# Optimization experiments

Measured on AMD Instinct MI355X. Metric: run time of the kernel, lower is better.

Reference implementation:

```python
import jax, jax.numpy as jnp
import numpy as np

CHANNELS, STYLE_DIM, N_HEADS, N_TOK = 512, 256, 2, 50
HEAD_DIM = STYLE_DIM // N_HEADS
SCALE = STYLE_DIM ** (-0.5)


def setup_inputs() -> dict:
    key = jax.random.key(0)
    ks = jax.random.split(key, 12)
    B, T = 16, 4096
    s = lambda fan_in: 1.0 / np.sqrt(fan_in)
    return {
        "x": jax.random.normal(ks[0], (B, CHANNELS, T), jnp.float32),
        "style": jax.random.normal(ks[1], (B, N_TOK, STYLE_DIM), jnp.float32),
        "key_emb": jax.random.normal(ks[2], (1, N_TOK, STYLE_DIM), jnp.float32) * 0.3,
        "Wq": jax.random.uniform(ks[3], (STYLE_DIM, CHANNELS), jnp.float32, -s(CHANNELS), s(CHANNELS)),
        "bq": jax.random.uniform(ks[4], (STYLE_DIM,), jnp.float32, -s(CHANNELS), s(CHANNELS)),
        "Wk": jax.random.uniform(ks[5], (STYLE_DIM, STYLE_DIM), jnp.float32, -s(STYLE_DIM), s(STYLE_DIM)),
        "bk": jax.random.uniform(ks[6], (STYLE_DIM,), jnp.float32, -s(STYLE_DIM), s(STYLE_DIM)),
        "Wv": jax.random.uniform(ks[7], (STYLE_DIM, STYLE_DIM), jnp.float32, -s(STYLE_DIM), s(STYLE_DIM)),
        "bv": jax.random.uniform(ks[8], (STYLE_DIM,), jnp.float32, -s(STYLE_DIM), s(STYLE_DIM)),
        "Wo": jax.random.uniform(ks[9], (CHANNELS, STYLE_DIM), jnp.float32, -s(STYLE_DIM), s(STYLE_DIM)),
        "bo": jax.random.uniform(ks[10], (CHANNELS,), jnp.float32, -s(STYLE_DIM), s(STYLE_DIM)),
    }


def reference(x, style, key_emb, Wq, bq, Wk, bk, Wv, bv, Wo, bo):
    B, C, T = x.shape
    N = style.shape[1]
    # Q from x (transposed to [B,T,C]); K from static learned embedding; V from style
    q = jnp.einsum('bct,dc->btd', x, Wq) + bq                 # [B,T,style_dim]
    k = jnp.einsum('bns,ds->bnd', jnp.broadcast_to(key_emb, (B, N_TOK, STYLE_DIM)), Wk) + bk
    v = jnp.einsum('bns,ds->bnd', style, Wv) + bv
    # split heads: [B,H,T,hd] / [B,H,N,hd]
    q = q.reshape(B, T, N_HEADS, HEAD_DIM).transpose(0, 2, 1, 3)
    k = k.reshape(B, N_TOK, N_HEADS, HEAD_DIM).transpose(0, 2, 1, 3)
    v = v.reshape(B, N, N_HEADS, HEAD_DIM).transpose(0, 2, 1, 3)
    # tanh applied to transposed keys before QK^T
    attn = jnp.einsum('bhtd,bhnd->bhtn', q, jnp.tanh(k)) * SCALE
    attn = jax.nn.softmax(attn, axis=-1)
    out = jnp.einsum('bhtn,bhnd->bhtd', attn, v)              # [B,H,T,hd]
    out = out.transpose(0, 2, 1, 3).reshape(B, T, STYLE_DIM)
    out = jnp.einsum('btd,cd->btc', out, Wo) + bo             # [B,T,C]
    return x + out.transpose(0, 2, 1)
```

## Files before the change

### kernel.cpp

```cpp
#include <hip/hip_runtime.h>
#include <stdint.h>

#define CHN 512
#define TDIM 4096
#define SD 256
#define HD 128
#define NTOK 50
#define NP 64
#define NB 16
#define TT 64
#define QPITCH 264
#define XPITCH 132
#define SCALE_ 0.0625f

typedef float f32x4 __attribute__((ext_vector_type(4)));
typedef unsigned int u32x4 __attribute__((ext_vector_type(4)));
typedef short s16x8 __attribute__((ext_vector_type(8)));

__device__ __forceinline__ uint16_t f2bf(float f) {
  union { float f; uint32_t u; } v; v.f = f;
  uint32_t r = (v.u + 0x7fffu + ((v.u >> 16) & 1u)) >> 16;
  return (uint16_t)r;
}
__device__ __forceinline__ uint32_t packbf(float lo, float hi) {
  return (uint32_t)f2bf(lo) | ((uint32_t)f2bf(hi) << 16);
}
__device__ __forceinline__ void mfma_bf16(f32x4& d, u32x4 a, u32x4 b) {
  union { u32x4 u; s16x8 s; } ua, ub;
  ua.u = a; ub.u = b;
  d = __builtin_amdgcn_mfma_f32_16x16x32_bf16(ua.s, ub.s, d, 0, 0, 0);
}

__global__ void conv_w_kernel(const float* __restrict__ Wq, const float* __restrict__ Wo,
                              uint16_t* __restrict__ wqb, uint16_t* __restrict__ wob) {
  int i = blockIdx.x * 256 + threadIdx.x;
  wqb[i] = f2bf(Wq[i]);
  wob[i] = f2bf(Wo[i]);
}

__global__ void prep_kv_kernel(const float* __restrict__ style, const float* __restrict__ kemb,
                               const float* __restrict__ Wk, const float* __restrict__ bk,
                               const float* __restrict__ Wv, const float* __restrict__ bv,
                               uint16_t* __restrict__ kt, uint16_t* __restrict__ vT) {
  int id = blockIdx.x * 256 + threadIdx.x;
  if (id < 2 * NP * HD) {
    int dh = id & (HD - 1);
    int n  = (id >> 7) & (NP - 1);
    int h  = id >> 13;
    uint16_t r = 0;
    if (n < NTOK) {
      int d = h * HD + dh;
      float acc = bk[d];
      const float* er = kemb + (size_t)n * SD;
      const float* wr = Wk + (size_t)d * SD;
      for (int s = 0; s < SD; s += 4) {
        float4 e = *(const float4*)(er + s);
        float4 w4 = *(const float4*)(wr + s);
        acc += e.x * w4.x + e.y * w4.y + e.z * w4.z + e.w * w4.w;
      }
      r = f2bf(tanhf(acc));
    }
    kt[id] = r;
  } else {
    int vid = id - 2 * NP * HD;
    int n  = vid & (NP - 1);
    int dh = (vid >> 6) & (HD - 1);
    int h  = (vid >> 13) & 1;
    int bb = vid >> 14;
    uint16_t r = 0;
    if (n < NTOK) {
      int d = h * HD + dh;
      float acc = bv[d];
      const float* sr = style + (size_t)(bb * NTOK + n) * SD;
      const float* wr = Wv + (size_t)d * SD;
      for (int s = 0; s < SD; s += 4) {
        float4 e = *(const float4*)(sr + s);
        float4 w4 = *(const float4*)(wr + s);
        acc += e.x * w4.x + e.y * w4.y + e.z * w4.z + e.w * w4.w;
      }
      r = f2bf(acc);
    }
    vT[vid] = r;
  }
}

__global__ __launch_bounds__(256, 2) void qproj_attn_kernel(
    const float* __restrict__ x, const float* __restrict__ bq,
    const uint16_t* __restrict__ wqb,
    const uint16_t* __restrict__ kt, const uint16_t* __restrict__ vT,
    uint16_t* __restrict__ o) {
  __shared__ uint16_t qs[TT * QPITCH];

  const int bb = blockIdx.y;
  const int t0 = blockIdx.x * TT;
  const int tid = threadIdx.x;
  const int lane = tid & 63;
  const int w = tid >> 6;
  const int l15 = lane & 15;
  const int g = lane >> 4;

  const float* xb = x + (size_t)bb * CHN * TDIM + t0;

  f32x4 acc[4][4];
#pragma unroll
  for (int mt = 0; mt < 4; ++mt)
#pragma unroll
    for (int nt = 0; nt < 4; ++nt) acc[mt][nt] = (f32x4){0.f, 0.f, 0.f, 0.f};

  const int tse = (tid & 31) << 1;
  const int cb  = (tid >> 5) << 1;

  float2 va[8], vb[8];
#pragma unroll
  for (int p = 0; p < 8; ++p) {
    int c = cb + 16 * p;
    va[p] = *(const float2*)(xb + (size_t)c * TDIM + tse);
    vb[p] = *(const float2*)(xb + (size_t)(c + 1) * TDIM + tse);
  }

  for (int cc = 0; cc < 4; ++cc) {
    const int c0 = cc * 128;
    __syncthreads();
#pragma unroll
    for (int p = 0; p < 8; ++p) {
      int cl = cb + 16 * p;
      *(uint32_t*)&qs[tse * XPITCH + cl]       = packbf(va[p].x, vb[p].x);
      *(uint32_t*)&qs[(tse + 1) * XPITCH + cl] = packbf(va[p].y, vb[p].y);
    }
    if (cc < 3) {
      const int c0n = c0 + 128;
#pragma unroll
      for (int p = 0; p < 8; ++p) {
        int c = c0n + cb + 16 * p;
        va[p] = *(const float2*)(xb + (size_t)c * TDIM + tse);
        vb[p] = *(const float2*)(xb + (size_t)(c + 1) * TDIM + tse);
      }
    }
    __syncthreads();
#pragma unroll
    for (int ks = 0; ks < 4; ++ks) {
      u32x4 afr[4];
#pragma unroll
      for (int mt = 0; mt < 4; ++mt) {
        int dr = (w * 4 + mt) * 16 + l15;
        afr[mt] = *(const u32x4*)(wqb + (size_t)dr * CHN + c0 + ks * 32 + g * 8);
      }
#pragma unroll
      for (int nt = 0; nt < 4; ++nt) {
        int tr = nt * 16 + l15;
        const uint16_t* pb = &qs[tr * XPITCH + ks * 32 + g * 8];
        uint2 lo = *(const uint2*)pb;
        uint2 hi = *(const uint2*)(pb + 4);
        u32x4 bfr = (u32x4){lo.x, lo.y, hi.x, hi.y};
#pragma unroll
        for (int mt = 0; mt < 4; ++mt) mfma_bf16(acc[mt][nt], afr[mt], bfr);
      }
    }
  }
  __syncthreads();
#pragma unroll
  for (int mt = 0; mt < 4; ++mt) {
    int d0 = (w * 4 + mt) * 16 + g * 4;
    float4 bqv = *(const float4*)(bq + d0);
#pragma unroll
    for (int nt = 0; nt < 4; ++nt) {
      int tr = nt * 16 + l15;
      uint2 wv;
      wv.x = packbf(acc[mt][nt][0] + bqv.x, acc[mt][nt][1] + bqv.y);
      wv.y = packbf(acc[mt][nt][2] + bqv.z, acc[mt][nt][3] + bqv.w);
      *(uint2*)&qs[tr * QPITCH + d0] = wv;
    }
  }
  __syncthreads();

  const int tmy = w * 16 + l15;
  const uint16_t* qrow = &qs[tmy * QPITCH];
  uint16_t* og = o + (size_t)(bb * TDIM + t0 + tmy) * SD;
  const int l1 = l15 + 16 * ((2 * g) & 3);
  const int l2 = l15 + 16 * ((2 * g + 1) & 3);
  const bool hiH = (g >> 1) != 0;

#pragma unroll
  for (int h = 0; h < 2; ++h) {
    u32x4 bq4[4];
#pragma unroll
    for (int ks = 0; ks < 4; ++ks)
      bq4[ks] = *(const u32x4*)(qrow + h * HD + ks * 32 + g * 8);

    f32x4 sac[4];
#pragma unroll
    for (int mtn = 0; mtn < 4; ++mtn) {
      sac[mtn] = (f32x4){0.f, 0.f, 0.f, 0.f};
#pragma unroll
      for (int ks = 0; ks < 4; ++ks) {
        u32x4 afr = *(const u32x4*)(kt + (size_t)(h * NP + mtn * 16 + l15) * HD + ks * 32 + g * 8);
        mfma_bf16(sac[mtn], afr, bq4[ks]);
      }
    }
    float pv[4][4];
    float mx = -3.0e38f;
#pragma unroll
    for (int mtn = 0; mtn < 4; ++mtn)
#pragma unroll
      for (int j = 0; j < 4; ++j) {
        int n = mtn * 16 + g * 4 + j;
        float s = (n < NTOK) ? sac[mtn][j] * SCALE_ : -3.0e38f;
        pv[mtn][j] = s;
        mx = fmaxf(mx, s);
      }
    mx = fmaxf(mx, __shfl_xor(mx, 16, 64));
    mx = fmaxf(mx, __shfl_xor(mx, 32, 64));
    float sum = 0.f;
#pragma unroll
    for (int mtn = 0; mtn < 4; ++mtn)
#pragma unroll
      for (int j = 0; j < 4; ++j) {
        float e = __expf(pv[mtn][j] - mx);
        pv[mtn][j] = e;
        sum += e;
      }
    sum += __shfl_xor(sum, 16, 64);
    sum += __shfl_xor(sum, 32, 64);
    float inv = 1.0f / sum;
    uint32_t pk[4][2];
#pragma unroll
    for (int mtn = 0; mtn < 4; ++mtn) {
      pk[mtn][0] = packbf(pv[mtn][0] * inv, pv[mtn][1] * inv);
      pk[mtn][1] = packbf(pv[mtn][2] * inv, pv[mtn][3] * inv);
    }
    u32x4 bp[2];
#pragma unroll
    for (int ks = 0; ks < 2; ++ks) {
      uint32_t a0 = (uint32_t)__shfl((int)pk[2 * ks][0], l1, 64);
      uint32_t b0 = (uint32_t)__shfl((int)pk[2 * ks + 1][0], l1, 64);
      uint32_t a1 = (uint32_t)__shfl((int)pk[2 * ks][1], l1, 64);
      uint32_t b1 = (uint32_t)__shfl((int)pk[2 * ks + 1][1], l1, 64);
      uint32_t a2 = (uint32_t)__shfl((int)pk[2 * ks][0], l2, 64);
      uint32_t b2 = (uint32_t)__shfl((int)pk[2 * ks + 1][0], l2, 64);
      uint32_t a3 = (uint32_t)__shfl((int)pk[2 * ks][1], l2, 64);
      uint32_t b3 = (uint32_t)__shfl((int)pk[2 * ks + 1][1], l2, 64);
      bp[ks] = (u32x4){hiH ? b0 : a0, hiH ? b1 : a1, hiH ? b2 : a2, hiH ? b3 : a3};
    }
    const uint16_t* vb2 = vT + (size_t)((bb * 2 + h) * HD) * NP;
#pragma unroll
    for (int mtd = 0; mtd < 8; ++mtd) {
      f32x4 oac = (f32x4){0.f, 0.f, 0.f, 0.f};
#pragma unroll
      for (int ks = 0; ks < 2; ++ks) {
        u32x4 afr = *(const u32x4*)(vb2 + (size_t)(mtd * 16 + l15) * NP + ks * 32 + g * 8);
        mfma_bf16(oac, afr, bp[ks]);
      }
      int d0 = h * HD + mtd * 16 + g * 4;
      uint2 wv;
      wv.x = packbf(oac[0], oac[1]);
      wv.y = packbf(oac[2], oac[3]);
      *(uint2*)(og + d0) = wv;
    }
  }
}

__global__ __launch_bounds__(256, 2) void oproj_kernel(
    const float* __restrict__ x, const float* __restrict__ bo,
    const uint16_t* __restrict__ wob, const uint16_t* __restrict__ o,
    float* __restrict__ out) {
  const int bb = blockIdx.y;
  const int t0 = blockIdx.x * TT;
  const int c0q = blockIdx.z * 128;
  const int tid = threadIdx.x;
  const int lane = tid & 63;
  const int w = tid >> 6;
  const int l15 = lane & 15;
  const int g = lane >> 4;
  const int tmy = w * 16 + l15;

  const uint16_t* orow_in = o + (size_t)(bb * TDIM + t0 + tmy) * SD;
  u32x4 ak[8];
#pragma unroll
  for (int ks = 0; ks < 8; ++ks)
    ak[ks] = *(const u32x4*)(orow_in + ks * 32 + g * 8);

  const float* xr = x + (size_t)bb * CHN * TDIM;
  float* orow = out + (size_t)bb * CHN * TDIM;
  const int t4 = t0 + w * 16 + g * 4;

#pragma unroll 4
  for (int nt = 0; nt < 8; ++nt) {
    int c = c0q + nt * 16 + l15;
    const uint16_t* wrow = wob + (size_t)c * SD;
    f32x4 yac = (f32x4){0.f, 0.f, 0.f, 0.f};
#pragma unroll
    for (int ks = 0; ks < 8; ++ks) {
      u32x4 bfr = *(const u32x4*)(wrow + ks * 32 + g * 8);
      mfma_bf16(yac, ak[ks], bfr);
    }
    float bov = bo[c];
    float4 xv = *(const float4*)(xr + (size_t)c * TDIM + t4);
    float4 ov;
    ov.x = xv.x + yac[0] + bov;
    ov.y = xv.y + yac[1] + bov;
    ov.z = xv.z + yac[2] + bov;
    ov.w = xv.w + yac[3] + bov;
    *(float4*)(orow + (size_t)c * TDIM + t4) = ov;
  }
}

extern "C" void kernel_launch(void* const* d_in, const int* in_sizes, int n_in,
                              void* d_out, int out_size, void* d_ws, size_t ws_size,
                              hipStream_t stream) {
  const float* x     = (const float*)d_in[0];
  const float* style = (const float*)d_in[1];
  const float* kemb  = (const float*)d_in[2];
  const float* Wq    = (const float*)d_in[3];
  const float* bq    = (const float*)d_in[4];
  const float* Wk    = (const float*)d_in[5];
  const float* bk    = (const float*)d_in[6];
  const float* Wv    = (const float*)d_in[7];
  const float* bv    = (const float*)d_in[8];
  const float* Wo    = (const float*)d_in[9];
  const float* bo    = (const float*)d_in[10];
  float* out = (float*)d_out;

  uint16_t* wqb = (uint16_t*)d_ws;
  uint16_t* wob = wqb + 131072;
  uint16_t* ktw = wob + 131072;
  uint16_t* vTw = ktw + 16384;
  uint16_t* ob  = vTw + 262144;

  conv_w_kernel<<<512, 256, 0, stream>>>(Wq, Wo, wqb, wob);
  prep_kv_kernel<<<1088, 256, 0, stream>>>(style, kemb, Wk, bk, Wv, bv, ktw, vTw);
  dim3 grid(TDIM / TT, NB);
  qproj_attn_kernel<<<grid, 256, 0, stream>>>(x, bq, wqb, ktw, vTw, ob);
  dim3 gridC(TDIM / TT, NB, 4);
  oproj_kernel<<<gridC, 256, 0, stream>>>(x, bo, wob, ob, out);
}
```

Measured before the change: 278.9 us.

## Restructure output projection with channel-major tiles and LDS-staged coalesced stores

The output projection kernel is reorganized so each block owns 16 output channels across 1024 timesteps, with Wo as the A operand and attention output rows as B. Accumulators are transposed through shared memory so each channel row of x and out is read and written as contiguous float4 runs along T, replacing the previous strided per-lane float4 accesses. In exchange, every block rereads the bf16 attention output (32x more reads of it overall) and adds two barriers per tile.

Result: no change. 283.3 us (+1.6%).

```diff
diff --git a/kernel.cpp b/kernel.cpp
--- a/kernel.cpp
+++ b/kernel.cpp
@@ -11,6 +11,7 @@
 #define TT 64
 #define QPITCH 264
 #define XPITCH 132
+#define YP 260
 #define SCALE_ 0.0625f
 
 typedef float f32x4 __attribute__((ext_vector_type(4)));
@@ -259,48 +260,69 @@
   }
 }
 
-__global__ __launch_bounds__(256, 2) void oproj_kernel(
+__global__ void oproj_kernel(
     const float* __restrict__ x, const float* __restrict__ bo,
     const uint16_t* __restrict__ wob, const uint16_t* __restrict__ o,
     float* __restrict__ out) {
+  __shared__ float ys[16 * YP];
+  const int c0 = blockIdx.x * 16;
   const int bb = blockIdx.y;
-  const int t0 = blockIdx.x * TT;
-  const int c0q = blockIdx.z * 128;
+  const int tq0 = blockIdx.z * 1024;
   const int tid = threadIdx.x;
   const int lane = tid & 63;
   const int w = tid >> 6;
   const int l15 = lane & 15;
   const int g = lane >> 4;
-  const int tmy = w * 16 + l15;
-
-  const uint16_t* orow_in = o + (size_t)(bb * TDIM + t0 + tmy) * SD;
-  u32x4 ak[8];
-#pragma unroll
-  for (int ks = 0; ks < 8; ++ks)
-    ak[ks] = *(const u32x4*)(orow_in + ks * 32 + g * 8);
-
-  const float* xr = x + (size_t)bb * CHN * TDIM;
-  float* orow = out + (size_t)bb * CHN * TDIM;
-  const int t4 = t0 + w * 16 + g * 4;
-
-#pragma unroll 4
-  for (int nt = 0; nt < 8; ++nt) {
-    int c = c0q + nt * 16 + l15;
-    const uint16_t* wrow = wob + (size_t)c * SD;
-    f32x4 yac = (f32x4){0.f, 0.f, 0.f, 0.f};
-#pragma unroll
-    for (int ks = 0; ks < 8; ++ks) {
-      u32x4 bfr = *(const u32x4*)(wrow + ks * 32 + g * 8);
-      mfma_bf16(yac, ak[ks], bfr);
-    }
-    float bov = bo[c];
-    float4 xv = *(const float4*)(xr + (size_t)c * TDIM + t4);
-    float4 ov;
-    ov.x = xv.x + yac[0] + bov;
-    ov.y = xv.y + yac[1] + bov;
-    ov.z = xv.z + yac[2] + bov;
-    ov.w = xv.w + yac[3] + bov;
-    *(float4*)(orow + (size_t)c * TDIM + t4) = ov;
+
+  const uint16_t* ob_ = o + (size_t)bb * TDIM * SD;
+  const float* xr = x + (size_t)(bb * CHN + c0) * TDIM;
+  float* our = out + (size_t)(bb * CHN + c0) * TDIM;
+
+  float4 bov = *(const float4*)(bo + c0 + w * 4);
+
+  for (int ti = 0; ti < 4; ++ti) {
+    const int tbase = tq0 + ti * 256;
+    f32x4 acc[4];
+#pragma unroll
+    for (int nt = 0; nt < 4; ++nt) acc[nt] = (f32x4){0.f, 0.f, 0.f, 0.f};
+#pragma unroll
+    for (int kh = 0; kh < 2; ++kh) {
+      u32x4 ak[4];
+#pragma unroll
+      for (int kk = 0; kk < 4; ++kk)
+        ak[kk] = *(const u32x4*)(wob + (size_t)(c0 + l15) * SD + (kh * 4 + kk) * 32 + g * 8);
+#pragma unroll
+      for (int nt = 0; nt < 4; ++nt) {
+        const uint16_t* orow = ob_ + (size_t)(tbase + w * 64 + nt * 16 + l15) * SD;
+#pragma unroll
+        for (int kk = 0; kk < 4; ++kk) {
+          u32x4 bfr = *(const u32x4*)(orow + (kh * 4 + kk) * 32 + g * 8);
+          mfma_bf16(acc[nt], ak[kk], bfr);
+        }
+      }
+    }
+    __syncthreads();
+#pragma unroll
+    for (int nt = 0; nt < 4; ++nt) {
+      int tl = w * 64 + nt * 16 + l15;
+#pragma unroll
+      for (int j = 0; j < 4; ++j)
+        ys[(g * 4 + j) * YP + tl] = acc[nt][j];
+    }
+    __syncthreads();
+#pragma unroll
+    for (int r = 0; r < 4; ++r) {
+      int cl = w * 4 + r;
+      float4 yv = *(float4*)&ys[cl * YP + lane * 4];
+      float4 xv = *(const float4*)(xr + (size_t)cl * TDIM + tbase + lane * 4);
+      float bb4 = (r == 0) ? bov.x : (r == 1) ? bov.y : (r == 2) ? bov.z : bov.w;
+      float4 ov;
+      ov.x = xv.x + yv.x + bb4;
+      ov.y = xv.y + yv.y + bb4;
+      ov.z = xv.z + yv.z + bb4;
+      ov.w = xv.w + yv.w + bb4;
+      *(float4*)(our + (size_t)cl * TDIM + tbase + lane * 4) = ov;
+    }
   }
 }
 
@@ -330,6 +352,6 @@
   prep_kv_kernel<<<1088, 256, 0, stream>>>(style, kemb, Wk, bk, Wv, bv, ktw, vTw);
   dim3 grid(TDIM / TT, NB);
   qproj_attn_kernel<<<grid, 256, 0, stream>>>(x, bq, wqb, ktw, vTw, ob);
-  dim3 gridC(TDIM / TT, NB, 4);
+  dim3 gridC(CHN / 16, NB, 4);
   oproj_kernel<<<gridC, 256, 0, stream>>>(x, bo, wob, ob, out);
 }
```
